# Optimization experiments

Hardware: AMD Instinct MI355X
Metric: run time of the kernel (lower is better)

## Reference

```python
import jax, jax.numpy as jnp
import numpy as np

H, DH, M, ITERS = 8, 64, 256, 6   # heads, dim_head, num_landmarks, pinv iters
DIM = H * DH                      # 512
KERNEL = 33                       # residual depthwise conv kernel


def setup_inputs() -> dict:
    key = jax.random.key(0)
    ks = jax.random.split(key, 5)
    b, n = 2, 8192                # n multiple of M -> no divisibility padding
    x = jax.random.normal(ks[0], (b, n, DIM), jnp.float32)
    ln_gamma = jnp.ones((DIM,), jnp.float32)
    ln_beta = jnp.zeros((DIM,), jnp.float32)
    w_qkv = jax.random.normal(ks[1], (DIM, 3 * DIM), jnp.float32) * 0.02
    w_out = jax.random.normal(ks[2], (DIM, DIM), jnp.float32) * 0.02
    b_out = jnp.zeros((DIM,), jnp.float32)
    res_kernel = jax.random.normal(ks[3], (H, 1, KERNEL, 1), jnp.float32) * 0.02
    return {"x": x, "ln_gamma": ln_gamma, "ln_beta": ln_beta, "w_qkv": w_qkv,
            "w_out": w_out, "b_out": b_out, "res_kernel": res_kernel}


def _pinv(a, iters):
    # lucidrains moore_penrose_iter_pinv (Newton-Schulz iteration)
    abs_a = jnp.abs(a)
    scale = abs_a.sum(-1).max() * abs_a.sum(-2).max()
    z = jnp.swapaxes(a, -1, -2) / scale
    I = jnp.eye(a.shape[-1], dtype=a.dtype)
    for _ in range(iters):
        az = a @ z
        z = 0.25 * z @ (13.0 * I - az @ (15.0 * I - az @ (7.0 * I - az)))
    return z


def reference(x, ln_gamma, ln_beta, w_qkv, w_out, b_out, res_kernel):
    b, n, d = x.shape
    # pre-LayerNorm (eps 1e-5)
    mu = jnp.mean(x, -1, keepdims=True)
    var = jnp.var(x, -1, keepdims=True)
    xn = (x - mu) * jax.lax.rsqrt(var + 1e-5) * ln_gamma + ln_beta
    # qkv projection (bias-free)
    q, k, v = jnp.split(xn @ w_qkv, 3, axis=-1)
    to_heads = lambda t: t.reshape(b, n, H, DH).transpose(0, 2, 1, 3)  # b h n d
    q, k, v = to_heads(q), to_heads(k), to_heads(v)
    q = q * (DH ** -0.5)
    # landmarks: mean over groups of l consecutive tokens ('(m l) d -> m d')
    l = n // M
    q_l = q.reshape(b, H, M, l, DH).mean(3)  # b h M d
    k_l = k.reshape(b, H, M, l, DH).mean(3)
    sim1 = jnp.einsum('bhnd,bhmd->bhnm', q, k_l)      # queries vs k-landmarks
    sim2 = jnp.einsum('bhid,bhjd->bhij', q_l, k_l)    # landmarks vs landmarks
    sim3 = jnp.einsum('bhmd,bhnd->bhmn', q_l, k)      # q-landmarks vs keys
    a1 = jax.nn.softmax(sim1, axis=-1)
    a2 = jax.nn.softmax(sim2, axis=-1)
    a3 = jax.nn.softmax(sim3, axis=-1)
    a2_inv = _pinv(a2, ITERS)
    out = (a1 @ a2_inv) @ (a3 @ v)  # b h n d
    # residual depthwise conv over the sequence axis (Conv2d kernel (33,1), groups=H)
    pad = KERNEL // 2
    out = out + jax.lax.conv_general_dilated(
        v, res_kernel, (1, 1), [(pad, pad), (0, 0)],
        dimension_numbers=('NCHW', 'OIHW', 'NCHW'), feature_group_count=H)
    out = out.transpose(0, 2, 1, 3).reshape(b, n, d)
    out = out @ w_out + b_out  # to_out Linear (dropout inactive at eval)
    return x + out             # TransLayer residual
```

## Files before the change

kernel.cpp:

```cpp
#include <hip/hip_runtime.h>
#include <math.h>

#define H_ 8
#define DH_ 64
#define DIM_ 512
#define M_ 256
#define N_ 8192
#define BH_ 16
#define LG_ 32
#define KC_ 33
#define CH_ 16
#define NTI_ 8

typedef __attribute__((ext_vector_type(8))) short bf16x8;
typedef __attribute__((ext_vector_type(4))) short s16x4;
typedef __attribute__((ext_vector_type(4))) float f32x4;

__device__ __forceinline__ short f2bf(float f) {
  unsigned u = __float_as_uint(f);
  unsigned r = (u + 0x7FFF + ((u >> 16) & 1)) >> 16;
  return (short)r;
}
__device__ __forceinline__ float bf2f(short s) {
  return __uint_as_float(((unsigned)(unsigned short)s) << 16);
}

__device__ __forceinline__ void mfma_nt_core(const short* __restrict__ A,
                                             const short* __restrict__ Bt, int K,
                                             int m0, int n0, size_t lda, size_t ldb,
                                             f32x4 acc[4][4], short* As, short* Bs) {
  const int tid = threadIdx.x;
  const int wave = tid >> 6, lane = tid & 63;
  const int wr = (wave >> 1) * 64, wc = (wave & 1) * 64;
  const int mi = lane & 15, quad = lane >> 4;
  for (int k0 = 0; k0 < K; k0 += 32) {
#pragma unroll
    for (int t = 0; t < 2; ++t) {
      const int cbase = (t * 4 + wave) * 64;
      const int chunk = cbase + lane;
      const int row = chunk >> 2, cc = (chunk & 3) * 8;
      __builtin_amdgcn_global_load_lds(
          (const __attribute__((address_space(1))) void*)(A + (size_t)(m0 + row) * lda + k0 + cc),
          (__attribute__((address_space(3))) void*)(As + (size_t)cbase * 8), 16, 0, 0);
      __builtin_amdgcn_global_load_lds(
          (const __attribute__((address_space(1))) void*)(Bt + (size_t)(n0 + row) * ldb + k0 + cc),
          (__attribute__((address_space(3))) void*)(Bs + (size_t)cbase * 8), 16, 0, 0);
    }
    __syncthreads();
    bf16x8 af[4], bf[4];
#pragma unroll
    for (int i = 0; i < 4; ++i)
      af[i] = *(const bf16x8*)&As[(wr + i * 16 + mi) * 32 + quad * 8];
#pragma unroll
    for (int j = 0; j < 4; ++j)
      bf[j] = *(const bf16x8*)&Bs[(wc + j * 16 + mi) * 32 + quad * 8];
#pragma unroll
    for (int i = 0; i < 4; ++i)
#pragma unroll
      for (int j = 0; j < 4; ++j)
        acc[i][j] = __builtin_amdgcn_mfma_f32_16x16x32_bf16(af[i], bf[j], acc[i][j], 0, 0, 0);
    __syncthreads();
  }
}

__global__ __launch_bounds__(256) void qkv_mfma(const short* __restrict__ xnb,
                                                const short* __restrict__ wt,
                                                short* __restrict__ qb, short* __restrict__ kb,
                                                short* __restrict__ vb) {
  __shared__ short As[128 * 32], Bs[128 * 32];
  f32x4 acc[4][4] = {};
  const int m0 = blockIdx.x * 128, n0 = blockIdx.y * 128;
  mfma_nt_core(xnb, wt, DIM_, m0, n0, DIM_, DIM_, acc, As, Bs);
  const int wave = threadIdx.x >> 6, lane = threadIdx.x & 63;
  const int wr = (wave >> 1) * 64, wc = (wave & 1) * 64;
  const int mi = lane & 15, quad = lane >> 4;
  const int which = n0 >> 9;
  short* dst = which == 0 ? qb : which == 1 ? kb : vb;
  const float sc = which == 0 ? 0.125f : 1.0f;
#pragma unroll
  for (int j = 0; j < 4; ++j) {
    const int col = n0 + wc + j * 16 + mi;
    const int h = (col >> 6) & 7, d = col & 63;
#pragma unroll
    for (int i = 0; i < 4; ++i) {
#pragma unroll
      for (int r = 0; r < 4; ++r) {
        const int row = m0 + wr + i * 16 + quad * 4 + r;
        const int b = row >> 13, t = row & (N_ - 1);
        dst[((size_t)(b * H_ + h) * N_ + t) * DH_ + d] = f2bf(acc[i][j][r] * sc);
      }
    }
  }
}

__global__ __launch_bounds__(256) void final_mfma(const short* __restrict__ omb,
                                                  const short* __restrict__ wt,
                                                  const float* __restrict__ x,
                                                  const float* __restrict__ bout,
                                                  float* __restrict__ y) {
  __shared__ short As[128 * 32], Bs[128 * 32];
  f32x4 acc[4][4] = {};
  const int m0 = blockIdx.x * 128, n0 = blockIdx.y * 128;
  mfma_nt_core(omb, wt, DIM_, m0, n0, DIM_, DIM_, acc, As, Bs);
  const int wave = threadIdx.x >> 6, lane = threadIdx.x & 63;
  const int wr = (wave >> 1) * 64, wc = (wave & 1) * 64;
  const int mi = lane & 15, quad = lane >> 4;
#pragma unroll
  for (int j = 0; j < 4; ++j) {
    const int col = n0 + wc + j * 16 + mi;
    const float bo = bout[col];
#pragma unroll
    for (int i = 0; i < 4; ++i) {
#pragma unroll
      for (int r = 0; r < 4; ++r) {
        const int row = m0 + wr + i * 16 + quad * 4 + r;
        y[(size_t)row * DIM_ + col] = acc[i][j][r] + x[(size_t)row * DIM_ + col] + bo;
      }
    }
  }
}

__global__ __launch_bounds__(256) void convt_kernel(const float* __restrict__ in,
                                                    short* __restrict__ out, int K, int N) {
  __shared__ float tile[32][33];
  const int n0 = blockIdx.x * 32, k0 = blockIdx.y * 32;
  const int tx = threadIdx.x & 31, ty = threadIdx.x >> 5;
  for (int r = ty; r < 32; r += 8) tile[r][tx] = in[(size_t)(k0 + r) * N + n0 + tx];
  __syncthreads();
  for (int r = ty; r < 32; r += 8) out[(size_t)(n0 + r) * K + k0 + tx] = f2bf(tile[tx][r]);
}

__global__ __launch_bounds__(256) void vt_kernel(const short* __restrict__ vb,
                                                 short* __restrict__ vtb) {
  __shared__ short tile[32][33];
  const int t0 = blockIdx.x * 32, d0 = blockIdx.y * 32, bh = blockIdx.z;
  const int tx = threadIdx.x & 31, ty = threadIdx.x >> 5;
  for (int r = ty; r < 32; r += 8)
    tile[r][tx] = vb[((size_t)bh * N_ + t0 + r) * DH_ + d0 + tx];
  __syncthreads();
  for (int r = ty; r < 32; r += 8)
    vtb[((size_t)bh * DH_ + d0 + r) * N_ + t0 + tx] = tile[tx][r];
}

__global__ __launch_bounds__(128) void ln_kernel(const float* __restrict__ x,
                                                 const float* __restrict__ gamma,
                                                 const float* __restrict__ beta,
                                                 short* __restrict__ xnb) {
  const int row = blockIdx.x, tid = threadIdx.x;
  const float4 v = ((const float4*)(x + (size_t)row * DIM_))[tid];
  float s = v.x + v.y + v.z + v.w;
  float ss = v.x * v.x + v.y * v.y + v.z * v.z + v.w * v.w;
  __shared__ float r1[128], r2[128];
  r1[tid] = s;
  r2[tid] = ss;
  __syncthreads();
  for (int off = 64; off > 0; off >>= 1) {
    if (tid < off) {
      r1[tid] += r1[tid + off];
      r2[tid] += r2[tid + off];
    }
    __syncthreads();
  }
  const float mu = r1[0] * (1.0f / DIM_);
  const float var = r2[0] * (1.0f / DIM_) - mu * mu;
  const float rs = rsqrtf(var + 1e-5f);
  const float4 g = ((const float4*)gamma)[tid];
  const float4 bb = ((const float4*)beta)[tid];
  s16x4 o = {f2bf((v.x - mu) * rs * g.x + bb.x), f2bf((v.y - mu) * rs * g.y + bb.y),
             f2bf((v.z - mu) * rs * g.z + bb.z), f2bf((v.w - mu) * rs * g.w + bb.w)};
  ((s16x4*)(xnb + (size_t)row * DIM_))[tid] = o;
}

__global__ __launch_bounds__(256) void landmark_kernel(const short* __restrict__ qb,
                                                       const short* __restrict__ kb,
                                                       float* __restrict__ ql,
                                                       float* __restrict__ kl,
                                                       short* __restrict__ qlb,
                                                       short* __restrict__ klb) {
  const int idx = blockIdx.x * 256 + threadIdx.x;
  const int d = idx & (DH_ - 1);
  const int m = (idx >> 6) & (M_ - 1);
  const int bh = idx >> 14;
  const size_t base = ((size_t)bh * N_ + m * LG_) * DH_ + d;
  float sq = 0.f, sk = 0.f;
#pragma unroll 8
  for (int t = 0; t < LG_; ++t) {
    sq += bf2f(qb[base + (size_t)t * DH_]);
    sk += bf2f(kb[base + (size_t)t * DH_]);
  }
  sq *= (1.0f / LG_);
  sk *= (1.0f / LG_);
  ql[idx] = sq;
  kl[idx] = sk;
  qlb[idx] = f2bf(sq);
  klb[idx] = f2bf(sk);
}

__global__ __launch_bounds__(256) void sim2_softmax(const float* __restrict__ ql,
                                                    const float* __restrict__ kl,
                                                    float* __restrict__ a2,
                                                    short* __restrict__ a2b) {
  const int i = blockIdx.x, bh = blockIdx.y, j = threadIdx.x;
  __shared__ float qrow[DH_];
  if (j < DH_) qrow[j] = ql[((size_t)bh * M_ + i) * DH_ + j];
  __syncthreads();
  const float* kr = kl + ((size_t)bh * M_ + j) * DH_;
  float s = 0.f;
#pragma unroll 16
  for (int d = 0; d < DH_; ++d) s += qrow[d] * kr[d];
  __shared__ float red[256];
  red[j] = s;
  __syncthreads();
  for (int off = 128; off > 0; off >>= 1) {
    if (j < off) red[j] = fmaxf(red[j], red[j + off]);
    __syncthreads();
  }
  const float mx = red[0];
  __syncthreads();
  const float e = expf(s - mx);
  red[j] = e;
  __syncthreads();
  for (int off = 128; off > 0; off >>= 1) {
    if (j < off) red[j] += red[j + off];
    __syncthreads();
  }
  const float out = e / red[0];
  a2[((size_t)bh * M_ + i) * M_ + j] = out;
  a2b[((size_t)bh * M_ + i) * M_ + j] = f2bf(out);
}

__global__ __launch_bounds__(256) void colmax_kernel(const float* __restrict__ a2,
                                                     unsigned int* __restrict__ scalebits) {
  const int bh = blockIdx.x, j = threadIdx.x;
  const float* mat = a2 + (size_t)bh * M_ * M_;
  float s = 0.f;
  for (int i = 0; i < M_; ++i) s += fabsf(mat[i * M_ + j]);
  __shared__ float red[256];
  red[j] = s;
  __syncthreads();
  for (int off = 128; off > 0; off >>= 1) {
    if (j < off) red[j] = fmaxf(red[j], red[j + off]);
    __syncthreads();
  }
  if (j == 0) atomicMax(scalebits, __float_as_uint(red[0]));
}

__global__ __launch_bounds__(256) void transpose_scale(const float* __restrict__ a2,
                                                       short* __restrict__ z0b,
                                                       const unsigned int* __restrict__ scalebits) {
  const float inv = 1.0f / __uint_as_float(*scalebits);
  const int idx = blockIdx.x * 256 + threadIdx.x;
  const int j = idx & (M_ - 1), i = (idx >> 8) & (M_ - 1), bh = idx >> 16;
  z0b[idx] = f2bf(a2[((size_t)bh * M_ + j) * M_ + i] * inv);
}

__device__ __forceinline__ void ns_core(const short* __restrict__ A, const short* __restrict__ B,
                                        int m0, int n0, short* As, short* Bs, f32x4 acc[4]) {
  const int tid = threadIdx.x, wave = tid >> 6, lane = tid & 63;
  const int mi = lane & 15, quad = lane >> 4;
  const int arow = tid >> 2, acol = (tid & 3) * 8;
  const int bkk = tid & 31, g = tid >> 5;
  for (int k0 = 0; k0 < M_; k0 += 32) {
    __builtin_amdgcn_global_load_lds(
        (const __attribute__((address_space(1))) void*)(A + (size_t)(m0 + arow) * M_ + k0 + acol),
        (__attribute__((address_space(3))) void*)(As + (size_t)wave * 512), 16, 0, 0);
    const bf16x8 bv = *(const bf16x8*)(B + (size_t)(k0 + bkk) * M_ + n0 + g * 8);
#pragma unroll
    for (int e = 0; e < 8; ++e) Bs[(g * 8 + e) * 44 + bkk] = bv[e];
    __syncthreads();
    const bf16x8 af = *(const bf16x8*)&As[(wave * 16 + mi) * 32 + quad * 8];
#pragma unroll
    for (int j = 0; j < 4; ++j) {
      union { bf16x8 v; s16x4 h[2]; } bfr;
      const short* bp = &Bs[(j * 16 + mi) * 44 + quad * 8];
      bfr.h[0] = *(const s16x4*)bp;
      bfr.h[1] = *(const s16x4*)(bp + 4);
      acc[j] = __builtin_amdgcn_mfma_f32_16x16x32_bf16(af, bfr.v, acc[j], 0, 0, 0);
    }
    __syncthreads();
  }
}

__device__ __forceinline__ int ns_remap() {
  const int lin = blockIdx.y * 16 + blockIdx.x;
  return (lin & 7) * (gridDim.y << 1) + (lin >> 3);
}

__global__ __launch_bounds__(256) void ns_gemm0(const short* __restrict__ A,
                                                const short* __restrict__ B,
                                                short* __restrict__ C) {
  __shared__ short As[64 * 32], Bs[64 * 44];
  const int id = ns_remap();
  const int bx = id & 15, by = id >> 4;
  const int m0 = (bx >> 2) * 64, n0 = (bx & 3) * 64;
  const size_t mo = (size_t)by * (M_ * M_);
  f32x4 acc[4] = {};
  ns_core(A + mo, B + mo, m0, n0, As, Bs, acc);
  const int wave = threadIdx.x >> 6, lane = threadIdx.x & 63;
  const int mi = lane & 15, quad = lane >> 4;
#pragma unroll
  for (int j = 0; j < 4; ++j)
#pragma unroll
    for (int r = 0; r < 4; ++r) {
      const int row = m0 + wave * 16 + quad * 4 + r, col = n0 + j * 16 + mi;
      C[mo + (size_t)row * M_ + col] = f2bf(acc[j][r]);
    }
}

__global__ __launch_bounds__(256) void ns_stageA(const short* __restrict__ z,
                                                 const short* __restrict__ y,
                                                 short* __restrict__ p1,
                                                 short* __restrict__ y2,
                                                 short* __restrict__ w) {
  __shared__ short As[64 * 32], Bs[64 * 44];
  const int id = ns_remap();
  const int bx = id & 15, by = id >> 4;
  const int m0 = (bx >> 2) * 64, n0 = (bx & 3) * 64;
  const int sel = by & 1;
  const size_t mo = (size_t)(by >> 1) * (M_ * M_);
  f32x4 acc[4] = {};
  ns_core((sel ? y : z) + mo, y + mo, m0, n0, As, Bs, acc);
  const int wave = threadIdx.x >> 6, lane = threadIdx.x & 63;
  const int mi = lane & 15, quad = lane >> 4;
#pragma unroll
  for (int j = 0; j < 4; ++j)
#pragma unroll
    for (int r = 0; r < 4; ++r) {
      const int row = m0 + wave * 16 + quad * 4 + r, col = n0 + j * 16 + mi;
      const size_t idx = mo + (size_t)row * M_ + col;
      if (sel) {
        y2[idx] = f2bf(acc[j][r]);
        w[idx] = f2bf(1.75f * bf2f(y[idx]) - 0.25f * acc[j][r]);
      } else {
        p1[idx] = f2bf(acc[j][r]);
      }
    }
}

__global__ __launch_bounds__(256) void ns_stageB(const short* __restrict__ p1,
                                                 const short* __restrict__ y2,
                                                 const short* __restrict__ w,
                                                 const short* __restrict__ z,
                                                 const short* __restrict__ y,
                                                 short* __restrict__ zo,
                                                 short* __restrict__ yo,
                                                 float* __restrict__ zf, int zonly) {
  __shared__ short As[64 * 32], Bs[64 * 44];
  const int id = ns_remap();
  const int bx = id & 15, by = id >> 4;
  const int m0 = (bx >> 2) * 64, n0 = (bx & 3) * 64;
  const int sel = zonly ? 0 : (by & 1);
  const size_t mo = (size_t)(zonly ? by : (by >> 1)) * (M_ * M_);
  f32x4 acc[4] = {};
  ns_core((sel ? y2 : p1) + mo, w + mo, m0, n0, As, Bs, acc);
  const int wave = threadIdx.x >> 6, lane = threadIdx.x & 63;
  const int mi = lane & 15, quad = lane >> 4;
#pragma unroll
  for (int j = 0; j < 4; ++j)
#pragma unroll
    for (int r = 0; r < 4; ++r) {
      const int row = m0 + wave * 16 + quad * 4 + r, col = n0 + j * 16 + mi;
      const size_t idx = mo + (size_t)row * M_ + col;
      if (sel) {
        yo[idx] = f2bf(3.25f * bf2f(y[idx]) - 3.75f * bf2f(y2[idx]) + acc[j][r]);
      } else {
        const float v = 3.25f * bf2f(z[idx]) - 3.75f * bf2f(p1[idx]) + acc[j][r];
        zo[idx] = f2bf(v);
        if (zf) zf[idx] = v;
      }
    }
}

__device__ __forceinline__ void mm_step(float (*As)[68], float (*Bs)[68],
                                        int tr, int tc, float acc[4][4]) {
#pragma unroll
  for (int kk = 0; kk < 16; ++kk) {
    const float4 a4 = *(const float4*)&As[kk][tr * 4];
    const float4 b4 = *(const float4*)&Bs[kk][tc * 4];
    const float a[4] = {a4.x, a4.y, a4.z, a4.w};
    const float b[4] = {b4.x, b4.y, b4.z, b4.w};
#pragma unroll
    for (int i = 0; i < 4; ++i)
#pragma unroll
      for (int j = 0; j < 4; ++j) acc[i][j] = fmaf(a[i], b[j], acc[i][j]);
  }
}

__device__ __forceinline__ void load_a_tile(const float* A, int lda, int m0, int k0,
                                            int tid, float (*As)[68]) {
  const int r = tid >> 2, kq = tid & 3;
  const float4 a4 = *(const float4*)(A + (size_t)(m0 + r) * lda + k0 + kq * 4);
  As[kq * 4 + 0][r] = a4.x;
  As[kq * 4 + 1][r] = a4.y;
  As[kq * 4 + 2][r] = a4.z;
  As[kq * 4 + 3][r] = a4.w;
}

__device__ __forceinline__ void load_b_nn(const float* B, int ldb, int k0, int n0,
                                          int tid, float (*Bs)[68]) {
  const int kr = tid >> 4, c4 = tid & 15;
  const float4 b4 = *(const float4*)(B + (size_t)(k0 + kr) * ldb + n0 + c4 * 4);
  *(float4*)&Bs[kr][c4 * 4] = b4;
}

__global__ __launch_bounds__(256) void gemm_nn64(const float* __restrict__ A, int lda,
                                                 long long strideA,
                                                 const float* __restrict__ B, long long strideB,
                                                 float* __restrict__ C, long long strideC,
                                                 int kchunk) {
  const int bz = blockIdx.z;
  A += (size_t)bz * strideA;
  B += (size_t)bz * strideB;
  C += (size_t)bz * strideC;
  const int m0 = blockIdx.x * 64;
  const int tid = threadIdx.x, tr = tid >> 4, tc = tid & 15;
  __shared__ float As[16][68], Bs[16][68];
  float acc[4][4] = {};
  for (int k0 = 0; k0 < kchunk; k0 += 16) {
    load_a_tile(A, lda, m0, k0, tid, As);
    load_b_nn(B, DH_, k0, 0, tid, Bs);
    __syncthreads();
    mm_step(As, Bs, tr, tc, acc);
    __syncthreads();
  }
#pragma unroll
  for (int i = 0; i < 4; ++i) {
    const int row = m0 + tr * 4 + i;
    *(float4*)(C + (size_t)row * DH_ + tc * 4) =
        make_float4(acc[i][0], acc[i][1], acc[i][2], acc[i][3]);
  }
}

__device__ __forceinline__ void stage_ks(const short* __restrict__ kb, int bh, int n0,
                                         int wave, int lane, short* ks) {
#pragma unroll
  for (int i = 0; i < 2; ++i) {
    const int cb = i * 256 + wave * 64;
    const int c = cb + lane;
    const int row = c >> 3, cc = c & 7;
    __builtin_amdgcn_global_load_lds(
        (const __attribute__((address_space(1))) void*)(
            kb + ((size_t)bh * N_ + n0 + row) * DH_ + ((cc ^ (row & 7)) * 8)),
        (__attribute__((address_space(3))) void*)(ks + (size_t)cb * 8), 16, 0, 0);
  }
}

__global__ __launch_bounds__(256) void a3_flash(const short* __restrict__ qlb,
                                                const short* __restrict__ kb,
                                                const short* __restrict__ vtb,
                                                float* __restrict__ Opart,
                                                float* __restrict__ mpart,
                                                float* __restrict__ lpart) {
  const int chunk = blockIdx.x, rt = blockIdx.y, bh = blockIdx.z;
  __shared__ short ks[64 * 64];
  __shared__ short ps[64 * 64];
  const int tid = threadIdx.x, wave = tid >> 6, lane = tid & 63;
  const int mi = lane & 15, quad = lane >> 4;
  const short* qrow = qlb + ((size_t)bh * M_ + rt * 64 + wave * 16 + mi) * DH_;
  const bf16x8 aq0 = *(const bf16x8*)(qrow + quad * 8);
  const bf16x8 aq1 = *(const bf16x8*)(qrow + 32 + quad * 8);
  float m[4] = {-INFINITY, -INFINITY, -INFINITY, -INFINITY};
  float l[4] = {0.f, 0.f, 0.f, 0.f};
  f32x4 o[4] = {};
  stage_ks(kb, bh, chunk * (N_ / CH_), wave, lane, ks);
  __syncthreads();
  for (int t = 0; t < NTI_; ++t) {
    const int n0 = chunk * (N_ / CH_) + t * 64;
    f32x4 s[4];
#pragma unroll
    for (int j = 0; j < 4; ++j) {
      const int row = j * 16 + mi;
      const bf16x8 b0 = *(const bf16x8*)&ks[row * 64 + ((quad ^ (row & 7)) * 8)];
      const bf16x8 b1 = *(const bf16x8*)&ks[row * 64 + (((quad + 4) ^ (row & 7)) * 8)];
      f32x4 z = {0.f, 0.f, 0.f, 0.f};
      z = __builtin_amdgcn_mfma_f32_16x16x32_bf16(aq0, b0, z, 0, 0, 0);
      s[j] = __builtin_amdgcn_mfma_f32_16x16x32_bf16(aq1, b1, z, 0, 0, 0);
    }
    __syncthreads();
    if (t + 1 < NTI_) stage_ks(kb, bh, n0 + 64, wave, lane, ks);
    float alpha[4];
#pragma unroll
    for (int r = 0; r < 4; ++r) {
      float v = fmaxf(fmaxf(s[0][r], s[1][r]), fmaxf(s[2][r], s[3][r]));
      v = fmaxf(v, __shfl_xor(v, 1, 64));
      v = fmaxf(v, __shfl_xor(v, 2, 64));
      v = fmaxf(v, __shfl_xor(v, 4, 64));
      v = fmaxf(v, __shfl_xor(v, 8, 64));
      const float mnew = fmaxf(m[r], v);
      alpha[r] = __expf(m[r] - mnew);
      m[r] = mnew;
    }
    float rs[4] = {0.f, 0.f, 0.f, 0.f};
#pragma unroll
    for (int j = 0; j < 4; ++j)
#pragma unroll
      for (int r = 0; r < 4; ++r) {
        const float p = __expf(s[j][r] - m[r]);
        rs[r] += p;
        const int prow = wave * 16 + quad * 4 + r;
        const int pcol = j * 16 + mi;
        ps[prow * 64 + (((pcol >> 3) ^ (prow & 7)) * 8) + (pcol & 7)] = f2bf(p);
      }
#pragma unroll
    for (int r = 0; r < 4; ++r) {
      float v = rs[r];
      v += __shfl_xor(v, 1, 64);
      v += __shfl_xor(v, 2, 64);
      v += __shfl_xor(v, 4, 64);
      v += __shfl_xor(v, 8, 64);
      l[r] = l[r] * alpha[r] + v;
#pragma unroll
      for (int j = 0; j < 4; ++j) o[j][r] *= alpha[r];
    }
    const int prow = wave * 16 + mi;
    const bf16x8 ap0 = *(const bf16x8*)&ps[prow * 64 + ((quad ^ (mi & 7)) * 8)];
    const bf16x8 ap1 = *(const bf16x8*)&ps[prow * 64 + (((quad + 4) ^ (mi & 7)) * 8)];
#pragma unroll
    for (int j = 0; j < 4; ++j) {
      const short* vp = vtb + ((size_t)bh * DH_ + j * 16 + mi) * N_ + n0;
      const bf16x8 b0 = *(const bf16x8*)(vp + quad * 8);
      const bf16x8 b1 = *(const bf16x8*)(vp + 32 + quad * 8);
      o[j] = __builtin_amdgcn_mfma_f32_16x16x32_bf16(ap0, b0, o[j], 0, 0, 0);
      o[j] = __builtin_amdgcn_mfma_f32_16x16x32_bf16(ap1, b1, o[j], 0, 0, 0);
    }
    __syncthreads();
  }
  const int p2 = bh * 4 + rt;
  float* Ob = Opart + ((size_t)chunk * 64 + p2) * 4096;
#pragma unroll
  for (int j = 0; j < 4; ++j)
#pragma unroll
    for (int r = 0; r < 4; ++r)
      Ob[(wave * 16 + quad * 4 + r) * 64 + j * 16 + mi] = o[j][r];
  if (mi == 0) {
#pragma unroll
    for (int r = 0; r < 4; ++r) {
      mpart[((size_t)chunk * 64 + p2) * 64 + wave * 16 + quad * 4 + r] = m[r];
      lpart[((size_t)chunk * 64 + p2) * 64 + wave * 16 + quad * 4 + r] = l[r];
    }
  }
}

__global__ __launch_bounds__(256) void a3_combine(const float* __restrict__ Opart,
                                                  const float* __restrict__ mpart,
                                                  const float* __restrict__ lpart,
                                                  float* __restrict__ a3v) {
  const int p2 = blockIdx.x, ds = blockIdx.y;
  const int bh = p2 >> 2, rt = p2 & 3;
  __shared__ float wgt[CH_][64];
  const int tid = threadIdx.x;
  if (tid < 64) {
    float mg = -INFINITY;
#pragma unroll
    for (int c = 0; c < CH_; ++c) mg = fmaxf(mg, mpart[((size_t)c * 64 + p2) * 64 + tid]);
    float e[CH_], lg = 0.f;
#pragma unroll
    for (int c = 0; c < CH_; ++c) {
      e[c] = __expf(mpart[((size_t)c * 64 + p2) * 64 + tid] - mg);
      lg += lpart[((size_t)c * 64 + p2) * 64 + tid] * e[c];
    }
    const float inv = 1.f / lg;
#pragma unroll
    for (int c = 0; c < CH_; ++c) wgt[c][tid] = e[c] * inv;
  }
  __syncthreads();
  for (int i = ds * 1024 + tid; i < ds * 1024 + 1024; i += 256) {
    const int row = i >> 6, d = i & 63;
    float s = 0.f;
#pragma unroll
    for (int c = 0; c < CH_; ++c) s += Opart[((size_t)c * 64 + p2) * 4096 + i] * wgt[c][row];
    a3v[((size_t)bh * M_ + rt * 64 + row) * DH_ + d] = s;
  }
}

__global__ __launch_bounds__(256) void w2t_kernel(const float* __restrict__ w2,
                                                  short* __restrict__ w2tb) {
  const int bh = blockIdx.x, tid = threadIdx.x;
  for (int i = tid; i < M_ * DH_; i += 256) {
    const int r = i >> 6, d = i & 63;
    w2tb[((size_t)bh * DH_ + d) * M_ + r] = f2bf(w2[(size_t)bh * M_ * DH_ + i]);
  }
}

__global__ __launch_bounds__(256) void a1_conv(const short* __restrict__ qb,
                                               const short* __restrict__ klb,
                                               const short* __restrict__ w2tb,
                                               const short* __restrict__ vtb,
                                               const float* __restrict__ rk,
                                               short* __restrict__ omb) {
  __shared__ __align__(16) char smem[20096];
  short* kls = (short*)smem;
  short* ps = (short*)smem;
  short* vwin = (short*)smem;
  short* band = (short*)(smem + 17920);
  const int bh = blockIdx.y, t0 = blockIdx.x * 64;
  const int b = bh >> 3, h = bh & 7;
  const int tid = threadIdx.x, wave = tid >> 6, lane = tid & 63;
  const int mi = lane & 15, quad = lane >> 4;

  const short* qrow = qb + ((size_t)bh * N_ + t0 + wave * 16 + mi) * DH_;
  const bf16x8 aq0 = *(const bf16x8*)(qrow + quad * 8);
  const bf16x8 aq1 = *(const bf16x8*)(qrow + 32 + quad * 8);

#pragma unroll
  for (int i = 0; i < 4; ++i) {
    const int idx = tid + i * 256;
    const int r = idx >> 6, c = idx & 63, u = c - r;
    band[r * 68 + c] = (u >= 0 && u < KC_) ? f2bf(rk[h * KC_ + u]) : (short)0;
  }

  float m[4] = {-INFINITY, -INFINITY, -INFINITY, -INFINITY};
  float l[4] = {0.f, 0.f, 0.f, 0.f};
  f32x4 o[4] = {};
#pragma unroll
  for (int half = 0; half < 2; ++half) {
    if (half) __syncthreads();
#pragma unroll
    for (int i = 0; i < 4; ++i) {
      const int cb = i * 256 + wave * 64;
      const int c = cb + lane;
      const int row = c >> 3, cc = c & 7;
      __builtin_amdgcn_global_load_lds(
          (const __attribute__((address_space(1))) void*)(
              klb + ((size_t)bh * M_ + half * 128 + row) * DH_ + (cc ^ (row & 7)) * 8),
          (__attribute__((address_space(3))) void*)(kls + (size_t)cb * 8), 16, 0, 0);
    }
    __syncthreads();
    f32x4 s[8];
#pragma unroll
    for (int f = 0; f < 8; ++f) {
      const int row = f * 16 + mi;
      const bf16x8 blo = *(const bf16x8*)&kls[row * 64 + ((quad ^ (row & 7)) * 8)];
      const bf16x8 bhi = *(const bf16x8*)&kls[row * 64 + (((quad + 4) ^ (row & 7)) * 8)];
      f32x4 z = {0.f, 0.f, 0.f, 0.f};
      z = __builtin_amdgcn_mfma_f32_16x16x32_bf16(aq0, blo, z, 0, 0, 0);
      s[f] = __builtin_amdgcn_mfma_f32_16x16x32_bf16(aq1, bhi, z, 0, 0, 0);
    }
    __syncthreads();
#pragma unroll
    for (int r = 0; r < 4; ++r) {
      float v = s[0][r];
#pragma unroll
      for (int f = 1; f < 8; ++f) v = fmaxf(v, s[f][r]);
      v = fmaxf(v, __shfl_xor(v, 1, 64));
      v = fmaxf(v, __shfl_xor(v, 2, 64));
      v = fmaxf(v, __shfl_xor(v, 4, 64));
      v = fmaxf(v, __shfl_xor(v, 8, 64));
      const float mnew = fmaxf(m[r], v);
      const float alpha = __expf(m[r] - mnew);
      m[r] = mnew;
      l[r] *= alpha;
#pragma unroll
      for (int j = 0; j < 4; ++j) o[j][r] *= alpha;
      float sum = 0.f;
#pragma unroll
      for (int f = 0; f < 8; ++f) {
        const float p = __expf(s[f][r] - mnew);
        s[f][r] = p;
        sum += p;
      }
      sum += __shfl_xor(sum, 1, 64);
      sum += __shfl_xor(sum, 2, 64);
      sum += __shfl_xor(sum, 4, 64);
      sum += __shfl_xor(sum, 8, 64);
      l[r] += sum;
    }
#pragma unroll
    for (int f = 0; f < 8; ++f)
#pragma unroll
      for (int r = 0; r < 4; ++r)
        ps[(wave * 16 + quad * 4 + r) * 140 + f * 16 + mi] = f2bf(s[f][r]);
#pragma unroll
    for (int k0 = 0; k0 < 4; ++k0) {
      union { bf16x8 v; s16x4 hh[2]; } ap;
      const short* pp = &ps[(wave * 16 + mi) * 140 + k0 * 32 + quad * 8];
      ap.hh[0] = *(const s16x4*)pp;
      ap.hh[1] = *(const s16x4*)(pp + 4);
#pragma unroll
      for (int j = 0; j < 4; ++j) {
        const bf16x8 bw = *(const bf16x8*)(w2tb + ((size_t)bh * DH_ + j * 16 + mi) * M_ +
                                           (half * 4 + k0) * 32 + quad * 8);
        o[j] = __builtin_amdgcn_mfma_f32_16x16x32_bf16(ap.v, bw, o[j], 0, 0, 0);
      }
    }
  }
  __syncthreads();

  {
    const int d = tid & 63, cg0 = tid >> 6;
    const short* vrow = vtb + ((size_t)bh * DH_ + d) * N_;
    for (int ch = cg0; ch < 14; ch += 4) {
      const int tbase = t0 - 16 + ch * 8;
      bf16x8 vv;
      if (tbase >= 0 && tbase + 8 <= N_) {
        vv = *(const bf16x8*)(vrow + tbase);
      } else {
#pragma unroll
        for (int e = 0; e < 8; ++e) {
          const int tt = tbase + e;
          vv[e] = (tt >= 0 && tt < N_) ? vrow[tt] : (short)0;
        }
      }
      *(bf16x8*)&vwin[d * 116 + ch * 8] = vv;
    }
  }
  __syncthreads();

#pragma unroll
  for (int r = 0; r < 4; ++r) {
    const float inv = 1.f / l[r];
#pragma unroll
    for (int j = 0; j < 4; ++j) o[j][r] *= inv;
  }

#pragma unroll
  for (int ks = 0; ks < 2; ++ks) {
    union { bf16x8 v; s16x4 hh[2]; } ab;
    const short* bp = &band[mi * 68 + ks * 32 + quad * 8];
    ab.hh[0] = *(const s16x4*)bp;
    ab.hh[1] = *(const s16x4*)(bp + 4);
#pragma unroll
    for (int j = 0; j < 4; ++j) {
      union { bf16x8 v; s16x4 hh[2]; } bv;
      const short* vp = &vwin[(j * 16 + mi) * 116 + wave * 16 + ks * 32 + quad * 8];
      bv.hh[0] = *(const s16x4*)vp;
      bv.hh[1] = *(const s16x4*)(vp + 4);
      o[j] = __builtin_amdgcn_mfma_f32_16x16x32_bf16(ab.v, bv.v, o[j], 0, 0, 0);
    }
  }
#pragma unroll
  for (int j = 0; j < 4; ++j) {
    const int d = j * 16 + mi;
#pragma unroll
    for (int r = 0; r < 4; ++r) {
      const int t = t0 + wave * 16 + quad * 4 + r;
      omb[((size_t)(b * N_ + t)) * DIM_ + h * DH_ + d] = f2bf(o[j][r]);
    }
  }
}

extern "C" void kernel_launch(void* const* d_in, const int* in_sizes, int n_in,
                              void* d_out, int out_size, void* d_ws, size_t ws_size,
                              hipStream_t stream) {
  (void)in_sizes; (void)n_in; (void)out_size;
  const float* x = (const float*)d_in[0];
  const float* gamma = (const float*)d_in[1];
  const float* beta = (const float*)d_in[2];
  const float* wqkv = (const float*)d_in[3];
  const float* wout = (const float*)d_in[4];
  const float* bout = (const float*)d_in[5];
  const float* rk = (const float*)d_in[6];
  float* y = (float*)d_out;
  float* ws = (float*)d_ws;

  size_t o = 0;
  short* xnb = (short*)(ws + o);   o += (size_t)2 * N_ * DIM_ / 2;
  short* wqkvt = (short*)(ws + o); o += (size_t)3 * DIM_ * DIM_ / 2;
  short* woutt = (short*)(ws + o); o += (size_t)DIM_ * DIM_ / 2;
  short* qb = (short*)(ws + o);    o += (size_t)BH_ * N_ * DH_ / 2;
  short* kb = (short*)(ws + o);    o += (size_t)BH_ * N_ * DH_ / 2;
  short* vb = (short*)(ws + o);    o += (size_t)BH_ * N_ * DH_ / 2;
  short* vtb = (short*)(ws + o);   o += (size_t)BH_ * N_ * DH_ / 2;
  float* ql = ws + o;  o += (size_t)BH_ * M_ * DH_;
  float* kl = ws + o;  o += (size_t)BH_ * M_ * DH_;
  short* qlb = (short*)(ws + o); o += (size_t)BH_ * M_ * DH_ / 2;
  short* klb = (short*)(ws + o); o += (size_t)BH_ * M_ * DH_ / 2;
  float* a2 = ws + o;  o += (size_t)BH_ * M_ * M_;
  float* z0f = ws + o; o += (size_t)BH_ * M_ * M_;
  short* a2b = (short*)(ws + o); o += (size_t)BH_ * M_ * M_ / 2;
  short* zb0 = (short*)(ws + o); o += (size_t)BH_ * M_ * M_ / 2;
  short* zb1 = (short*)(ws + o); o += (size_t)BH_ * M_ * M_ / 2;
  short* yb0 = (short*)(ws + o); o += (size_t)BH_ * M_ * M_ / 2;
  short* yb1 = (short*)(ws + o); o += (size_t)BH_ * M_ * M_ / 2;
  short* p1b = (short*)(ws + o); o += (size_t)BH_ * M_ * M_ / 2;
  short* y2b = (short*)(ws + o); o += (size_t)BH_ * M_ * M_ / 2;
  short* wb  = (short*)(ws + o); o += (size_t)BH_ * M_ * M_ / 2;
  float* Opart = ws + o; o += (size_t)CH_ * 64 * 4096;
  float* mpart = ws + o; o += (size_t)CH_ * 64 * 64;
  float* lpart = ws + o; o += (size_t)CH_ * 64 * 64;
  float* a3v = ws + o; o += (size_t)BH_ * M_ * DH_;
  float* w2 = ws + o;  o += (size_t)BH_ * M_ * DH_;
  short* w2tb = (short*)(ws + o); o += (size_t)BH_ * M_ * DH_ / 2;
  short* omb = (short*)(ws + o);  o += (size_t)2 * N_ * DIM_ / 2;
  unsigned int* scalebits = (unsigned int*)(ws + o); o += 16;
  if (ws_size < o * sizeof(float)) return;

  (void)hipMemsetAsync(scalebits, 0, 64, stream);
  ln_kernel<<<2 * N_, 128, 0, stream>>>(x, gamma, beta, xnb);
  convt_kernel<<<dim3(3 * DIM_ / 32, DIM_ / 32), 256, 0, stream>>>(wqkv, wqkvt, DIM_, 3 * DIM_);
  convt_kernel<<<dim3(DIM_ / 32, DIM_ / 32), 256, 0, stream>>>(wout, woutt, DIM_, DIM_);
  qkv_mfma<<<dim3(2 * N_ / 128, 3 * DIM_ / 128), 256, 0, stream>>>(xnb, wqkvt, qb, kb, vb);
  vt_kernel<<<dim3(N_ / 32, 2, BH_), 256, 0, stream>>>(vb, vtb);

  landmark_kernel<<<BH_ * M_ * DH_ / 256, 256, 0, stream>>>(qb, kb, ql, kl, qlb, klb);
  sim2_softmax<<<dim3(M_, BH_), 256, 0, stream>>>(ql, kl, a2, a2b);
  colmax_kernel<<<BH_, 256, 0, stream>>>(a2, scalebits);
  transpose_scale<<<BH_ * M_ * M_ / 256, 256, 0, stream>>>(a2, zb0, scalebits);

  a3_flash<<<dim3(CH_, 4, BH_), 256, 0, stream>>>(qlb, kb, vtb, Opart, mpart, lpart);
  a3_combine<<<dim3(64, 4), 256, 0, stream>>>(Opart, mpart, lpart, a3v);

  ns_gemm0<<<dim3(16, BH_), 256, 0, stream>>>(a2b, zb0, yb0);
  short* zc = zb0; short* zn = zb1; short* yc = yb0; short* yn = yb1;
  for (int it = 0; it < 6; ++it) {
    const int last = (it == 5);
    ns_stageA<<<dim3(16, 2 * BH_), 256, 0, stream>>>(zc, yc, p1b, y2b, wb);
    ns_stageB<<<dim3(16, last ? BH_ : 2 * BH_), 256, 0, stream>>>(
        p1b, y2b, wb, zc, yc, zn, yn, last ? z0f : nullptr, last);
    short* t;
    t = zc; zc = zn; zn = t;
    t = yc; yc = yn; yn = t;
  }

  gemm_nn64<<<dim3(M_ / 64, 1, BH_), 256, 0, stream>>>(
      z0f, M_, (long long)M_ * M_, a3v, (long long)M_ * DH_, w2, (long long)M_ * DH_, M_);
  w2t_kernel<<<BH_, 256, 0, stream>>>(w2, w2tb);

  a1_conv<<<dim3(N_ / 64, BH_), 256, 0, stream>>>(qb, klb, w2tb, vtb, rk, omb);

  final_mfma<<<dim3(2 * N_ / 128, DIM_ / 128), 256, 0, stream>>>(omb, woutt, x, bout, y);
}
```

Measured before the change: 469.7 us.

## Read k-landmarks directly from global in a1_conv and prefetch V window early

The a1_conv kernel no longer stages k-landmark tiles into shared memory with async global-to-LDS loads. Each wave now reads its MFMA operands directly from global memory, which relies on L2/L1 caching and removes several block-wide barriers. The V window load for the residual conv moves to the kernel start so it overlaps with the attention work, and the softmax P tile is written to LDS in two 64-column chunks per wave to shrink the staging buffer. The shared buffers are no longer aliased, so total LDS use per block grows, which may reduce occupancy. The K reads also lose the XOR-swizzled, coalesced LDS path.

```diff
diff --git a/kernel.cpp b/kernel.cpp
--- a/kernel.cpp
+++ b/kernel.cpp
@@ -588,11 +588,9 @@
                                                const short* __restrict__ vtb,
                                                const float* __restrict__ rk,
                                                short* __restrict__ omb) {
-  __shared__ __align__(16) char smem[20096];
-  short* kls = (short*)smem;
-  short* ps = (short*)smem;
-  short* vwin = (short*)smem;
-  short* band = (short*)(smem + 17920);
+  __shared__ short ps[64 * 76];
+  __shared__ short vwin[64 * 116];
+  __shared__ short band[16 * 68];
   const int bh = blockIdx.y, t0 = blockIdx.x * 64;
   const int b = bh >> 3, h = bh & 7;
   const int tid = threadIdx.x, wave = tid >> 6, lane = tid & 63;
@@ -602,6 +600,24 @@
   const bf16x8 aq0 = *(const bf16x8*)(qrow + quad * 8);
   const bf16x8 aq1 = *(const bf16x8*)(qrow + 32 + quad * 8);
 
+  {
+    const int d = tid & 63, cg0 = tid >> 6;
+    const short* vrow = vtb + ((size_t)bh * DH_ + d) * N_;
+    for (int ch = cg0; ch < 14; ch += 4) {
+      const int tbase = t0 - 16 + ch * 8;
+      bf16x8 vv;
+      if (tbase >= 0 && tbase + 8 <= N_) {
+        vv = *(const bf16x8*)(vrow + tbase);
+      } else {
+#pragma unroll
+        for (int e = 0; e < 8; ++e) {
+          const int tt = tbase + e;
+          vv[e] = (tt >= 0 && tt < N_) ? vrow[tt] : (short)0;
+        }
+      }
+      *(bf16x8*)&vwin[d * 116 + ch * 8] = vv;
+    }
+  }
 #pragma unroll
   for (int i = 0; i < 4; ++i) {
     const int idx = tid + i * 256;
@@ -614,29 +630,16 @@
   f32x4 o[4] = {};
 #pragma unroll
   for (int half = 0; half < 2; ++half) {
-    if (half) __syncthreads();
-#pragma unroll
-    for (int i = 0; i < 4; ++i) {
-      const int cb = i * 256 + wave * 64;
-      const int c = cb + lane;
-      const int row = c >> 3, cc = c & 7;
-      __builtin_amdgcn_global_load_lds(
-          (const __attribute__((address_space(1))) void*)(
-              klb + ((size_t)bh * M_ + half * 128 + row) * DH_ + (cc ^ (row & 7)) * 8),
-          (__attribute__((address_space(3))) void*)(kls + (size_t)cb * 8), 16, 0, 0);
-    }
-    __syncthreads();
     f32x4 s[8];
 #pragma unroll
     for (int f = 0; f < 8; ++f) {
-      const int row = f * 16 + mi;
-      const bf16x8 blo = *(const bf16x8*)&kls[row * 64 + ((quad ^ (row & 7)) * 8)];
-      const bf16x8 bhi = *(const bf16x8*)&kls[row * 64 + (((quad + 4) ^ (row & 7)) * 8)];
+      const short* kr = klb + ((size_t)bh * M_ + half * 128 + f * 16 + mi) * DH_;
+      const bf16x8 blo = *(const bf16x8*)(kr + quad * 8);
+      const bf16x8 bhi = *(const bf16x8*)(kr + 32 + quad * 8);
       f32x4 z = {0.f, 0.f, 0.f, 0.f};
       z = __builtin_amdgcn_mfma_f32_16x16x32_bf16(aq0, blo, z, 0, 0, 0);
       s[f] = __builtin_amdgcn_mfma_f32_16x16x32_bf16(aq1, bhi, z, 0, 0, 0);
     }
-    __syncthreads();
 #pragma unroll
     for (int r = 0; r < 4; ++r) {
       float v = s[0][r];
@@ -666,42 +669,25 @@
       l[r] += sum;
     }
 #pragma unroll
-    for (int f = 0; f < 8; ++f)
-#pragma unroll
-      for (int r = 0; r < 4; ++r)
-        ps[(wave * 16 + quad * 4 + r) * 140 + f * 16 + mi] = f2bf(s[f][r]);
-#pragma unroll
-    for (int k0 = 0; k0 < 4; ++k0) {
-      union { bf16x8 v; s16x4 hh[2]; } ap;
-      const short* pp = &ps[(wave * 16 + mi) * 140 + k0 * 32 + quad * 8];
-      ap.hh[0] = *(const s16x4*)pp;
-      ap.hh[1] = *(const s16x4*)(pp + 4);
-#pragma unroll
-      for (int j = 0; j < 4; ++j) {
-        const bf16x8 bw = *(const bf16x8*)(w2tb + ((size_t)bh * DH_ + j * 16 + mi) * M_ +
-                                           (half * 4 + k0) * 32 + quad * 8);
-        o[j] = __builtin_amdgcn_mfma_f32_16x16x32_bf16(ap.v, bw, o[j], 0, 0, 0);
-      }
-    }
-  }
-  __syncthreads();
-
-  {
-    const int d = tid & 63, cg0 = tid >> 6;
-    const short* vrow = vtb + ((size_t)bh * DH_ + d) * N_;
-    for (int ch = cg0; ch < 14; ch += 4) {
-      const int tbase = t0 - 16 + ch * 8;
-      bf16x8 vv;
-      if (tbase >= 0 && tbase + 8 <= N_) {
-        vv = *(const bf16x8*)(vrow + tbase);
-      } else {
-#pragma unroll
-        for (int e = 0; e < 8; ++e) {
-          const int tt = tbase + e;
-          vv[e] = (tt >= 0 && tt < N_) ? vrow[tt] : (short)0;
+    for (int sub = 0; sub < 2; ++sub) {
+#pragma unroll
+      for (int f = 0; f < 4; ++f)
+#pragma unroll
+        for (int r = 0; r < 4; ++r)
+          ps[(wave * 16 + quad * 4 + r) * 76 + f * 16 + mi] = f2bf(s[sub * 4 + f][r]);
+#pragma unroll
+      for (int k0 = 0; k0 < 2; ++k0) {
+        union { bf16x8 v; s16x4 hh[2]; } ap;
+        const short* pp = &ps[(wave * 16 + mi) * 76 + k0 * 32 + quad * 8];
+        ap.hh[0] = *(const s16x4*)pp;
+        ap.hh[1] = *(const s16x4*)(pp + 4);
+#pragma unroll
+        for (int j = 0; j < 4; ++j) {
+          const bf16x8 bw = *(const bf16x8*)(w2tb + ((size_t)bh * DH_ + j * 16 + mi) * M_ +
+                                             half * 128 + sub * 64 + k0 * 32 + quad * 8);
+          o[j] = __builtin_amdgcn_mfma_f32_16x16x32_bf16(ap.v, bw, o[j], 0, 0, 0);
         }
       }
-      *(bf16x8*)&vwin[d * 116 + ch * 8] = vv;
     }
   }
   __syncthreads();
```

Result: slower. 484.4 us (+3.1%).

## Load full-K tiles in Newton-Schulz GEMMs; use two-pass softmax in a1_conv

Applied to the files above, without the earlier changes.

The Newton-Schulz GEMM core now loads the whole K=256 slice of B into shared memory in one step and keeps the A fragments in registers. This removes the per-32-K loop with two barriers per iteration. Separately, a1_conv keeps all 256 landmark scores in registers and computes an exact max and sum before the P@W2 product, which drops the online-softmax rescaling. It also sets an occupancy hint of 5 blocks per SM. The cost is more LDS per NS block (about 33KB) and more registers, and the launch bound may force spills in a1_conv.

```diff
diff --git a/kernel.cpp b/kernel.cpp
--- a/kernel.cpp
+++ b/kernel.cpp
@@ -255,29 +255,35 @@
 }
 
 __device__ __forceinline__ void ns_core(const short* __restrict__ A, const short* __restrict__ B,
-                                        int m0, int n0, short* As, short* Bs, f32x4 acc[4]) {
+                                        int m0, int n0, short* Bs, f32x4 acc[4]) {
   const int tid = threadIdx.x, wave = tid >> 6, lane = tid & 63;
   const int mi = lane & 15, quad = lane >> 4;
-  const int arow = tid >> 2, acol = (tid & 3) * 8;
   const int bkk = tid & 31, g = tid >> 5;
-  for (int k0 = 0; k0 < M_; k0 += 32) {
-    __builtin_amdgcn_global_load_lds(
-        (const __attribute__((address_space(1))) void*)(A + (size_t)(m0 + arow) * M_ + k0 + acol),
-        (__attribute__((address_space(3))) void*)(As + (size_t)wave * 512), 16, 0, 0);
-    const bf16x8 bv = *(const bf16x8*)(B + (size_t)(k0 + bkk) * M_ + n0 + g * 8);
-#pragma unroll
-    for (int e = 0; e < 8; ++e) Bs[(g * 8 + e) * 44 + bkk] = bv[e];
-    __syncthreads();
-    const bf16x8 af = *(const bf16x8*)&As[(wave * 16 + mi) * 32 + quad * 8];
+  bf16x8 bv[8];
+#pragma unroll
+  for (int kc = 0; kc < 8; ++kc)
+    bv[kc] = *(const bf16x8*)(B + (size_t)(kc * 32 + bkk) * M_ + n0 + g * 8);
+  const short* arow = A + (size_t)(m0 + wave * 16 + mi) * M_;
+  bf16x8 af[8];
+#pragma unroll
+  for (int k0 = 0; k0 < 8; ++k0)
+    af[k0] = *(const bf16x8*)(arow + k0 * 32 + quad * 8);
+#pragma unroll
+  for (int kc = 0; kc < 8; ++kc)
+#pragma unroll
+    for (int e = 0; e < 8; ++e)
+      Bs[(g * 8 + e) * 260 + kc * 32 + bkk] = bv[kc][e];
+  __syncthreads();
+#pragma unroll
+  for (int k0 = 0; k0 < 8; ++k0) {
 #pragma unroll
     for (int j = 0; j < 4; ++j) {
       union { bf16x8 v; s16x4 h[2]; } bfr;
-      const short* bp = &Bs[(j * 16 + mi) * 44 + quad * 8];
+      const short* bp = &Bs[(j * 16 + mi) * 260 + k0 * 32 + quad * 8];
       bfr.h[0] = *(const s16x4*)bp;
       bfr.h[1] = *(const s16x4*)(bp + 4);
-      acc[j] = __builtin_amdgcn_mfma_f32_16x16x32_bf16(af, bfr.v, acc[j], 0, 0, 0);
-    }
-    __syncthreads();
+      acc[j] = __builtin_amdgcn_mfma_f32_16x16x32_bf16(af[k0], bfr.v, acc[j], 0, 0, 0);
+    }
   }
 }
 
@@ -289,13 +295,13 @@
 __global__ __launch_bounds__(256) void ns_gemm0(const short* __restrict__ A,
                                                 const short* __restrict__ B,
                                                 short* __restrict__ C) {
-  __shared__ short As[64 * 32], Bs[64 * 44];
+  __shared__ short Bs[64 * 260];
   const int id = ns_remap();
   const int bx = id & 15, by = id >> 4;
   const int m0 = (bx >> 2) * 64, n0 = (bx & 3) * 64;
   const size_t mo = (size_t)by * (M_ * M_);
   f32x4 acc[4] = {};
-  ns_core(A + mo, B + mo, m0, n0, As, Bs, acc);
+  ns_core(A + mo, B + mo, m0, n0, Bs, acc);
   const int wave = threadIdx.x >> 6, lane = threadIdx.x & 63;
   const int mi = lane & 15, quad = lane >> 4;
 #pragma unroll
@@ -312,14 +318,14 @@
                                                  short* __restrict__ p1,
                                                  short* __restrict__ y2,
                                                  short* __restrict__ w) {
-  __shared__ short As[64 * 32], Bs[64 * 44];
+  __shared__ short Bs[64 * 260];
   const int id = ns_remap();
   const int bx = id & 15, by = id >> 4;
   const int m0 = (bx >> 2) * 64, n0 = (bx & 3) * 64;
   const int sel = by & 1;
   const size_t mo = (size_t)(by >> 1) * (M_ * M_);
   f32x4 acc[4] = {};
-  ns_core((sel ? y : z) + mo, y + mo, m0, n0, As, Bs, acc);
+  ns_core((sel ? y : z) + mo, y + mo, m0, n0, Bs, acc);
   const int wave = threadIdx.x >> 6, lane = threadIdx.x & 63;
   const int mi = lane & 15, quad = lane >> 4;
 #pragma unroll
@@ -345,14 +351,14 @@
                                                  short* __restrict__ zo,
                                                  short* __restrict__ yo,
                                                  float* __restrict__ zf, int zonly) {
-  __shared__ short As[64 * 32], Bs[64 * 44];
+  __shared__ short Bs[64 * 260];
   const int id = ns_remap();
   const int bx = id & 15, by = id >> 4;
   const int m0 = (bx >> 2) * 64, n0 = (bx & 3) * 64;
   const int sel = zonly ? 0 : (by & 1);
   const size_t mo = (size_t)(zonly ? by : (by >> 1)) * (M_ * M_);
   f32x4 acc[4] = {};
-  ns_core((sel ? y2 : p1) + mo, w + mo, m0, n0, As, Bs, acc);
+  ns_core((sel ? y2 : p1) + mo, w + mo, m0, n0, Bs, acc);
   const int wave = threadIdx.x >> 6, lane = threadIdx.x & 63;
   const int mi = lane & 15, quad = lane >> 4;
 #pragma unroll
@@ -582,12 +588,12 @@
   }
 }
 
-__global__ __launch_bounds__(256) void a1_conv(const short* __restrict__ qb,
-                                               const short* __restrict__ klb,
-                                               const short* __restrict__ w2tb,
-                                               const short* __restrict__ vtb,
-                                               const float* __restrict__ rk,
-                                               short* __restrict__ omb) {
+__global__ __launch_bounds__(256, 5) void a1_conv(const short* __restrict__ qb,
+                                                  const short* __restrict__ klb,
+                                                  const short* __restrict__ w2tb,
+                                                  const short* __restrict__ vtb,
+                                                  const float* __restrict__ rk,
+                                                  short* __restrict__ omb) {
   __shared__ __align__(16) char smem[20096];
   short* kls = (short*)smem;
   short* ps = (short*)smem;
@@ -609,9 +615,7 @@
     band[r * 68 + c] = (u >= 0 && u < KC_) ? f2bf(rk[h * KC_ + u]) : (short)0;
   }
 
-  float m[4] = {-INFINITY, -INFINITY, -INFINITY, -INFINITY};
-  float l[4] = {0.f, 0.f, 0.f, 0.f};
-  f32x4 o[4] = {};
+  f32x4 s[16] = {};
 #pragma unroll
   for (int half = 0; half < 2; ++half) {
     if (half) __syncthreads();
@@ -626,50 +630,48 @@
           (__attribute__((address_space(3))) void*)(kls + (size_t)cb * 8), 16, 0, 0);
     }
     __syncthreads();
-    f32x4 s[8];
 #pragma unroll
     for (int f = 0; f < 8; ++f) {
       const int row = f * 16 + mi;
       const bf16x8 blo = *(const bf16x8*)&kls[row * 64 + ((quad ^ (row & 7)) * 8)];
       const bf16x8 bhi = *(const bf16x8*)&kls[row * 64 + (((quad + 4) ^ (row & 7)) * 8)];
-      f32x4 z = {0.f, 0.f, 0.f, 0.f};
-      z = __builtin_amdgcn_mfma_f32_16x16x32_bf16(aq0, blo, z, 0, 0, 0);
-      s[f] = __builtin_amdgcn_mfma_f32_16x16x32_bf16(aq1, bhi, z, 0, 0, 0);
-    }
-    __syncthreads();
-#pragma unroll
-    for (int r = 0; r < 4; ++r) {
-      float v = s[0][r];
-#pragma unroll
-      for (int f = 1; f < 8; ++f) v = fmaxf(v, s[f][r]);
-      v = fmaxf(v, __shfl_xor(v, 1, 64));
-      v = fmaxf(v, __shfl_xor(v, 2, 64));
-      v = fmaxf(v, __shfl_xor(v, 4, 64));
-      v = fmaxf(v, __shfl_xor(v, 8, 64));
-      const float mnew = fmaxf(m[r], v);
-      const float alpha = __expf(m[r] - mnew);
-      m[r] = mnew;
-      l[r] *= alpha;
-#pragma unroll
-      for (int j = 0; j < 4; ++j) o[j][r] *= alpha;
-      float sum = 0.f;
-#pragma unroll
-      for (int f = 0; f < 8; ++f) {
-        const float p = __expf(s[f][r] - mnew);
-        s[f][r] = p;
-        sum += p;
-      }
-      sum += __shfl_xor(sum, 1, 64);
-      sum += __shfl_xor(sum, 2, 64);
-      sum += __shfl_xor(sum, 4, 64);
-      sum += __shfl_xor(sum, 8, 64);
-      l[r] += sum;
-    }
+      f32x4 z = __builtin_amdgcn_mfma_f32_16x16x32_bf16(aq0, blo, s[half * 8 + f], 0, 0, 0);
+      s[half * 8 + f] = __builtin_amdgcn_mfma_f32_16x16x32_bf16(aq1, bhi, z, 0, 0, 0);
+    }
+  }
+  float inv[4];
+#pragma unroll
+  for (int r = 0; r < 4; ++r) {
+    float v = s[0][r];
+#pragma unroll
+    for (int f = 1; f < 16; ++f) v = fmaxf(v, s[f][r]);
+    v = fmaxf(v, __shfl_xor(v, 1, 64));
+    v = fmaxf(v, __shfl_xor(v, 2, 64));
+    v = fmaxf(v, __shfl_xor(v, 4, 64));
+    v = fmaxf(v, __shfl_xor(v, 8, 64));
+    float sum = 0.f;
+#pragma unroll
+    for (int f = 0; f < 16; ++f) {
+      const float p = __expf(s[f][r] - v);
+      s[f][r] = p;
+      sum += p;
+    }
+    sum += __shfl_xor(sum, 1, 64);
+    sum += __shfl_xor(sum, 2, 64);
+    sum += __shfl_xor(sum, 4, 64);
+    sum += __shfl_xor(sum, 8, 64);
+    inv[r] = 1.f / sum;
+  }
+  __syncthreads();
+
+  f32x4 o[4] = {};
+#pragma unroll
+  for (int half = 0; half < 2; ++half) {
 #pragma unroll
     for (int f = 0; f < 8; ++f)
 #pragma unroll
       for (int r = 0; r < 4; ++r)
-        ps[(wave * 16 + quad * 4 + r) * 140 + f * 16 + mi] = f2bf(s[f][r]);
+        ps[(wave * 16 + quad * 4 + r) * 140 + f * 16 + mi] = f2bf(s[half * 8 + f][r] * inv[r]);
 #pragma unroll
     for (int k0 = 0; k0 < 4; ++k0) {
       union { bf16x8 v; s16x4 hh[2]; } ap;
@@ -705,13 +707,6 @@
     }
   }
   __syncthreads();
-
-#pragma unroll
-  for (int r = 0; r < 4; ++r) {
-    const float inv = 1.f / l[r];
-#pragma unroll
-    for (int j = 0; j < 4; ++j) o[j][r] *= inv;
-  }
 
 #pragma unroll
   for (int ks = 0; ks < 2; ++ks) {
```

Result: no change. 463.9 us (-1.2%).
